# Optimization experiments

Measured on AMD Instinct MI355X. Metric: run time of the kernel, lower is better.

## Reference

```python
import jax, jax.numpy as jnp
import numpy as np

D_LATENT, D_HIDDEN, D_TIME, K = 128, 256, 16, 3
B, NX = 8, 4096
MSG_IN = 2 * D_LATENT + 1 + D_TIME + 2  # 275
UPD_IN = 2 * D_LATENT + D_TIME          # 272


def _gelu(v):
    return jax.nn.gelu(v, approximate=False)  # torch nn.GELU default (erf)


def _linear_params(key, din, dout):
    k1, k2 = jax.random.split(key)
    bound = 1.0 / np.sqrt(din)
    w = jax.random.uniform(k1, (din, dout), minval=-bound, maxval=bound, dtype=jnp.float32)
    b = jax.random.uniform(k2, (dout,), minval=-bound, maxval=bound, dtype=jnp.float32)
    return w, b


def setup_inputs() -> dict:
    key = jax.random.key(0)
    ks = jax.random.split(key, 16)
    inp = {
        'h': jax.random.normal(ks[0], (B, NX, D_LATENT), dtype=jnp.float32),
        'x': jax.random.uniform(ks[1], (B, NX), dtype=jnp.float32),
        'tau': jax.random.normal(ks[2], (B, D_TIME), dtype=jnp.float32),
        'u0': jax.random.normal(ks[3], (B, NX), dtype=jnp.float32),
    }
    inp['msg_w1'], inp['msg_b1'] = _linear_params(ks[4], MSG_IN, D_HIDDEN)
    inp['msg_w2'], inp['msg_b2'] = _linear_params(ks[5], D_HIDDEN, D_HIDDEN)
    inp['msg_w3'], inp['msg_b3'] = _linear_params(ks[6], D_HIDDEN, D_LATENT)
    inp['gate_w1'], inp['gate_b1'] = _linear_params(ks[7], MSG_IN, D_HIDDEN)
    inp['gate_w2'], inp['gate_b2'] = _linear_params(ks[8], D_HIDDEN, 1)
    inp['upd_w1'], inp['upd_b1'] = _linear_params(ks[9], UPD_IN, D_HIDDEN)
    inp['upd_w2'], inp['upd_b2'] = _linear_params(ks[10], D_HIDDEN, D_HIDDEN)
    inp['upd_w3'], inp['upd_b3'] = _linear_params(ks[11], D_HIDDEN, D_LATENT)
    inp['W_w'], inp['W_b'] = _linear_params(ks[12], D_LATENT, D_LATENT)
    return inp


def reference(h, x, tau, u0, msg_w1, msg_b1, msg_w2, msg_b2, msg_w3, msg_b3,
              gate_w1, gate_b1, gate_w2, gate_b2,
              upd_w1, upd_b1, upd_w2, upd_b2, upd_w3, upd_b3, W_w, W_b):
    Bq, nx, d = h.shape
    k = K
    S = 2 * k + 1
    # replicate padding along the spatial dim
    h_pad = jnp.pad(h, ((0, 0), (k, k), (0, 0)), mode='edge')
    x_pad = jnp.pad(x, ((0, 0), (k, k)), mode='edge')
    u0_pad = jnp.pad(u0, ((0, 0), (k, k)), mode='edge')
    # all stencil windows at once: idx[nx, S] gathers neighbor j for node i
    idx = jnp.arange(nx)[:, None] + jnp.arange(S)[None, :]
    h_j = h_pad[:, idx, :]                                  # [B, nx, S, d]
    rel = (x_pad[:, idx] - x[:, :, None])[..., None]        # [B, nx, S, 1]
    du0 = (u0[:, :, None] - u0_pad[:, idx])[..., None]      # [B, nx, S, 1]
    h_e = jnp.broadcast_to(h[:, :, None, :], (Bq, nx, S, d))
    tau_e = jnp.broadcast_to(tau[:, None, None, :], (Bq, nx, S, tau.shape[-1]))
    msg_in = jnp.concatenate([h_e, h_j, rel, tau_e, du0, jnp.abs(du0)], axis=-1)  # [B,nx,S,275]
    a = _gelu(msg_in @ msg_w1 + msg_b1)
    a = _gelu(a @ msg_w2 + msg_b2)
    msg = a @ msg_w3 + msg_b3                               # [B, nx, S, d]
    g = _gelu(msg_in @ gate_w1 + gate_b1)
    gate = jax.nn.sigmoid(g @ gate_w2 + gate_b2)            # [B, nx, S, 1]
    agg = jnp.sum(gate * msg, axis=2)                       # [B, nx, d]
    tau_n = jnp.broadcast_to(tau[:, None, :], (Bq, nx, tau.shape[-1]))
    upd_in = jnp.concatenate([h, agg, tau_n], axis=-1)      # [B, nx, 272]
    u = _gelu(upd_in @ upd_w1 + upd_b1)
    u = _gelu(u @ upd_w2 + upd_b2)
    h_nonlocal = u @ upd_w3 + upd_b3
    h_local = h @ W_w + W_b
    return _gelu(h_nonlocal + h_local)
```

## Files before the change

kernel.cpp:

```cpp
#include <hip/hip_runtime.h>
#include <hip/hip_bf16.h>
#include <math.h>

#define NXC 4096
#define NNODES 32768

typedef __attribute__((ext_vector_type(8))) short bf16x8;
typedef __attribute__((ext_vector_type(4))) short s16x4;
typedef __attribute__((ext_vector_type(16))) float f32x16;

#define MFMA32(a,b,c) __builtin_amdgcn_mfma_f32_32x32x16_bf16((a),(b),(c),0,0,0)

__device__ __forceinline__ float gelu_f(float v) {
    float z = v * fmaf(v*v, 0.10294324f, 2.3022082f);
    float e = __builtin_amdgcn_exp2f(z);
    return v - v * __builtin_amdgcn_rcpf(1.0f + e);
}
__device__ __forceinline__ float sigmoid_f(float v) {
    float e = __builtin_amdgcn_exp2f(-1.4426950409f * v);
    return __builtin_amdgcn_rcpf(1.0f + e);
}
__device__ __forceinline__ short f2bs(float x) {
    __hip_bfloat16 b = __float2bfloat16(x);
    union { __hip_bfloat16 h; short s; } u; u.h = b; return u.s;
}
__device__ __forceinline__ f32x16 zero16() {
    f32x16 v;
    #pragma unroll
    for (int i = 0; i < 16; ++i) v[i] = 0.f;
    return v;
}

__global__ void tau_kernel(const float* __restrict__ tau,
                           const float* __restrict__ msg_w1, const float* __restrict__ msg_b1,
                           const float* __restrict__ gate_w1, const float* __restrict__ gate_b1,
                           const float* __restrict__ upd_w1, const float* __restrict__ upd_b1,
                           float* __restrict__ TM, float* __restrict__ TG, float* __restrict__ TU)
{
    const int b = blockIdx.x;
    const int t = threadIdx.x;
    float tv[16];
    #pragma unroll
    for (int k = 0; k < 16; ++k) tv[k] = tau[b*16 + k];
    float am = msg_b1[t], ag = gate_b1[t], au = upd_b1[t];
    #pragma unroll
    for (int k = 0; k < 16; ++k) {
        am = fmaf(tv[k], msg_w1 [(257+k)*256 + t], am);
        ag = fmaf(tv[k], gate_w1[(257+k)*256 + t], ag);
        au = fmaf(tv[k], upd_w1 [(256+k)*256 + t], au);
    }
    TM[b*256+t] = am; TG[b*256+t] = ag; TU[b*256+t] = au;
}

__global__ void wconv_kernel(const float* __restrict__ msg_w2, const float* __restrict__ msg_w3,
                             const float* __restrict__ msg_w1, const float* __restrict__ gate_w1,
                             const float* __restrict__ upd_w1, const float* __restrict__ upd_w2,
                             const float* __restrict__ upd_w3, const float* __restrict__ W_w,
                             __hip_bfloat16* __restrict__ w2t, __hip_bfloat16* __restrict__ w3t,
                             __hip_bfloat16* __restrict__ wall_t, __hip_bfloat16* __restrict__ w1bt,
                             __hip_bfloat16* __restrict__ w2ut, __hip_bfloat16* __restrict__ w3ut)
{
    int i = blockIdx.x * 256 + threadIdx.x;
    if (i < 65536) { int c=i>>8, k=i&255; w2t[i] = __float2bfloat16(msg_w2[k*256+c]); return; }
    i -= 65536;
    if (i < 32768) { int c=i>>8, k=i&255; w3t[i] = __float2bfloat16(msg_w3[k*128+c]); return; }
    i -= 32768;
    if (i < 180224) {
        int c = i>>7, k = i&127; float v;
        if      (c <  256) v = msg_w1 [k*256 + c];
        else if (c <  512) v = msg_w1 [(128+k)*256 + (c-256)];
        else if (c <  768) v = gate_w1[k*256 + (c-512)];
        else if (c < 1024) v = gate_w1[(128+k)*256 + (c-768)];
        else if (c < 1280) v = upd_w1 [k*256 + (c-1024)];
        else               v = W_w    [k*128 + (c-1280)];
        wall_t[i] = __float2bfloat16(v); return;
    }
    i -= 180224;
    if (i < 32768) { int c=i>>7, k=i&127; w1bt[i] = __float2bfloat16(upd_w1[(128+k)*256+c]); return; }
    i -= 32768;
    if (i < 65536) { int c=i>>8, k=i&255; w2ut[i] = __float2bfloat16(upd_w2[k*256+c]); return; }
    i -= 65536;
    { int c=i>>8, k=i&255; w3ut[i] = __float2bfloat16(upd_w3[k*128+c]); }
}

#define PSTR 136

__global__ __launch_bounds__(256, 4)
void precompute_kernel(const float* __restrict__ h, const __hip_bfloat16* __restrict__ wall_t,
                       const float* __restrict__ W_b,
                       __hip_bfloat16* __restrict__ PAm, __hip_bfloat16* __restrict__ PBm,
                       __hip_bfloat16* __restrict__ PAg, __hip_bfloat16* __restrict__ PBg,
                       __hip_bfloat16* __restrict__ HU, float* __restrict__ HL)
{
    __shared__ __align__(16) __hip_bfloat16 hs[64*PSTR];
    const int t = threadIdx.x;
    const int lane = t & 63, wv = t >> 6;
    const int cl = lane & 31, g = lane >> 5;
    const int base = blockIdx.x * 64;
    const int tile = blockIdx.y;

    #pragma unroll
    for (int i = 0; i < 8; ++i) {
        int f = (i*256 + t)*4;
        float4 hv = *(const float4*)&h[(size_t)base*128 + f];
        int row = f >> 7, col = f & 127;
        s16x4 pk; pk[0]=f2bs(hv.x); pk[1]=f2bs(hv.y); pk[2]=f2bs(hv.z); pk[3]=f2bs(hv.w);
        *(s16x4*)&hs[row*PSTR + col] = pk;
    }
    __syncthreads();

    f32x16 acc0 = zero16(), acc1 = zero16();
    {
        const __hip_bfloat16* wp  = wall_t + ((size_t)tile*128 + wv*32 + cl)*128 + g*8;
        const __hip_bfloat16* a0  = hs + (size_t)(cl)*PSTR + g*8;
        const __hip_bfloat16* a1p = hs + (size_t)(32+cl)*PSTR + g*8;
        #pragma unroll
        for (int kt = 0; kt < 8; ++kt) {
            bf16x8 bf = *(const bf16x8*)(wp + kt*16);
            acc0 = MFMA32(*(const bf16x8*)(a0  + kt*16), bf, acc0);
            acc1 = MFMA32(*(const bf16x8*)(a1p + kt*16), bf, acc1);
        }
    }
    if (tile < 10) {
        __syncthreads();
        __hip_bfloat16* ob = hs;
        const int ncol = wv*32 + cl;
        #pragma unroll
        for (int r = 0; r < 16; ++r) {
            int row = (r&3) + 8*(r>>2) + 4*g;
            ob[row*128 + ncol]      = __float2bfloat16(acc0[r]);
            ob[(32+row)*128 + ncol] = __float2bfloat16(acc1[r]);
        }
        __syncthreads();
        __hip_bfloat16* bufs[5] = {PAm, PBm, PAg, PBg, HU};
        __hip_bfloat16* dst = bufs[tile >> 1];
        const int coloff = (tile & 1) * 128;
        #pragma unroll
        for (int i = 0; i < 4; ++i) {
            int idx = i*256 + t;
            int row = idx >> 4, ch = idx & 15;
            *(float4*)&dst[(size_t)(base+row)*256 + coloff + ch*8] =
                *(const float4*)&ob[row*128 + ch*8];
        }
    } else {
        const int col = (wv*32 + cl) & 127;
        float wb = W_b[col];
        #pragma unroll
        for (int r = 0; r < 16; ++r) {
            int row = (r&3) + 8*(r>>2) + 4*g;
            HL[(size_t)(base+row)*128 + col]    = acc0[r] + wb;
            HL[(size_t)(base+32+row)*128 + col] = acc1[r] + wb;
        }
    }
}

#define ENPB 8
#define EEPB 56
#define ARS  264
#define MRS  132

__global__ __launch_bounds__(256, 4)
void edge_kernel(const float* __restrict__ x, const float* __restrict__ u0,
                 const float* __restrict__ msg_w1, const float* __restrict__ gate_w1,
                 const __hip_bfloat16* __restrict__ w2t, const float* __restrict__ msg_b2,
                 const __hip_bfloat16* __restrict__ w3t, const float* __restrict__ msg_b3,
                 const float* __restrict__ gate_w2, const float* __restrict__ gate_b2,
                 const __hip_bfloat16* __restrict__ PAm, const __hip_bfloat16* __restrict__ PBm,
                 const __hip_bfloat16* __restrict__ PAg, const __hip_bfloat16* __restrict__ PBg,
                 const float* __restrict__ TM, const float* __restrict__ TG,
                 float* __restrict__ AGG)
{
    __shared__ __align__(16) __hip_bfloat16 act[64*ARS];
    __shared__ float s_gp[4][EEPB];
    __shared__ float s_rel[EEPB], s_du[EEPB], s_ad[EEPB];
    __shared__ int   s_slotj[14];
    __shared__ float s_gate[EEPB];

    const int t    = threadIdx.x;
    const int lane = t & 63;
    const int wv   = t >> 6;
    const int base = blockIdx.x * ENPB;
    const int b    = base >> 12;
    const int ii0  = base & (NXC-1);

    if (t < 14) {
        int jj = ii0 - 3 + t;
        jj = jj < 0 ? 0 : (jj > NXC-1 ? NXC-1 : jj);
        s_slotj[t] = b*NXC + jj;
    }
    if (t < EEPB) {
        int nd = t / 7, s = t - nd*7;
        int i  = base + nd;
        int jj = ii0 + nd + s - 3;
        jj = jj < 0 ? 0 : (jj > NXC-1 ? NXC-1 : jj);
        int j = b*NXC + jj;
        float rel = x[j] - x[i];
        float du  = u0[i] - u0[j];
        s_rel[t] = rel; s_du[t] = du; s_ad[t] = fabsf(du);
    }
    __syncthreads();

    {
        float wr  = msg_w1 [256*256+t], wd  = msg_w1 [273*256+t], wa  = msg_w1 [274*256+t];
        float gwr = gate_w1[256*256+t], gwd = gate_w1[273*256+t], gwa = gate_w1[274*256+t];
        float tm = TM[b*256+t], tg = TG[b*256+t];
        float g2 = gate_w2[t];
        float bm[14], bg[14], pam[8], pag[8];
        #pragma unroll
        for (int q = 0; q < 14; ++q) {
            size_t o = (size_t)s_slotj[q]*256 + t;
            bm[q] = __bfloat162float(PBm[o]) + tm;
            bg[q] = __bfloat162float(PBg[o]) + tg;
        }
        #pragma unroll
        for (int nd = 0; nd < 8; ++nd) {
            size_t o = (size_t)(base+nd)*256 + t;
            pam[nd] = __bfloat162float(PAm[o]);
            pag[nd] = __bfloat162float(PAg[o]);
        }
        #pragma unroll
        for (int nd = 0; nd < 8; ++nd) {
            #pragma unroll
            for (int s = 0; s < 7; ++s) {
                const int e = nd*7 + s, q = nd + s;
                float rel = s_rel[e], du = s_du[e], ad = s_ad[e];
                float pm = pam[nd] + bm[q];
                pm = fmaf(rel, wr, pm); pm = fmaf(du, wd, pm); pm = fmaf(ad, wa, pm);
                act[e*ARS + t] = __float2bfloat16(gelu_f(pm));
                float pg = pag[nd] + bg[q];
                pg = fmaf(rel, gwr, pg); pg = fmaf(du, gwd, pg); pg = fmaf(ad, gwa, pg);
                float gv = gelu_f(pg) * g2;
                #pragma unroll
                for (int off = 32; off > 0; off >>= 1) gv += __shfl_xor(gv, off);
                if (lane == 0) s_gp[wv][e] = gv;
            }
        }
    }
    __syncthreads();
    if (t < EEPB)
        s_gate[t] = sigmoid_f(s_gp[0][t] + s_gp[1][t] + s_gp[2][t] + s_gp[3][t] + gate_b2[0]);

    const int cl = lane & 31;
    const int g  = lane >> 5;
    f32x16 acc00 = zero16(), acc01 = zero16(), acc10 = zero16(), acc11 = zero16();
    {
        const __hip_bfloat16* w2a = w2t + (size_t)((wv*2+0)*32 + cl)*256 + g*8;
        const __hip_bfloat16* w2b = w2t + (size_t)((wv*2+1)*32 + cl)*256 + g*8;
        const __hip_bfloat16* a1a = act + (size_t)(cl)*ARS + g*8;
        const __hip_bfloat16* a1b = act + (size_t)(32+cl)*ARS + g*8;
        #pragma unroll
        for (int kt = 0; kt < 16; ++kt) {
            bf16x8 bfa = *(const bf16x8*)(w2a + kt*16);
            bf16x8 bfb = *(const bf16x8*)(w2b + kt*16);
            bf16x8 afa = *(const bf16x8*)(a1a + kt*16);
            bf16x8 afb = *(const bf16x8*)(a1b + kt*16);
            acc00 = MFMA32(afa, bfa, acc00);
            acc01 = MFMA32(afa, bfb, acc01);
            acc10 = MFMA32(afb, bfa, acc10);
            acc11 = MFMA32(afb, bfb, acc11);
        }
    }
    __syncthreads();
    {
        const int c0 = (wv*2+0)*32 + cl;
        const int c1 = (wv*2+1)*32 + cl;
        float b20 = msg_b2[c0], b21 = msg_b2[c1];
        #pragma unroll
        for (int r = 0; r < 16; ++r) {
            int row0 = (r&3) + 8*(r>>2) + 4*g;
            int row1 = 32 + row0;
            act[row0*ARS + c0] = __float2bfloat16(gelu_f(acc00[r] + b20));
            act[row0*ARS + c1] = __float2bfloat16(gelu_f(acc01[r] + b21));
            act[row1*ARS + c0] = __float2bfloat16(gelu_f(acc10[r] + b20));
            act[row1*ARS + c1] = __float2bfloat16(gelu_f(acc11[r] + b21));
        }
    }
    __syncthreads();

    f32x16 m0 = zero16(), m1 = zero16();
    {
        const __hip_bfloat16* w3p = w3t + (size_t)(wv*32 + cl)*256 + g*8;
        const __hip_bfloat16* a2a = act + (size_t)(cl)*ARS + g*8;
        const __hip_bfloat16* a2b = act + (size_t)(32+cl)*ARS + g*8;
        #pragma unroll
        for (int kt = 0; kt < 16; ++kt) {
            bf16x8 bfr = *(const bf16x8*)(w3p + kt*16);
            m0 = MFMA32(*(const bf16x8*)(a2a + kt*16), bfr, m0);
            m1 = MFMA32(*(const bf16x8*)(a2b + kt*16), bfr, m1);
        }
    }
    __syncthreads();
    float* msgbuf = (float*)act;
    {
        const int c = wv*32 + cl;
        float b3v = msg_b3[c];
        #pragma unroll
        for (int r = 0; r < 16; ++r) {
            int row0 = (r&3) + 8*(r>>2) + 4*g;
            int row1 = 32 + row0;
            msgbuf[row0*MRS + c] = (m0[r] + b3v) * s_gate[row0];
            if (row1 < EEPB)
                msgbuf[row1*MRS + c] = (m1[r] + b3v) * s_gate[row1];
        }
    }
    __syncthreads();

    {
        const int c   = t & 127;
        const int grp = t >> 7;
        #pragma unroll
        for (int p = 0; p < 4; ++p) {
            int nd = grp + p*2;
            float ssum = 0.f;
            #pragma unroll
            for (int q2 = 0; q2 < 7; ++q2) ssum += msgbuf[(nd*7+q2)*MRS + c];
            AGG[(size_t)(base+nd)*128 + c] = ssum;
        }
    }
}

#define UM 32

__global__ __launch_bounds__(256, 4)
void update_kernel(const __hip_bfloat16* __restrict__ w1bt, const __hip_bfloat16* __restrict__ w2ut,
                   const __hip_bfloat16* __restrict__ w3ut,
                   const float* __restrict__ upd_b2, const float* __restrict__ upd_b3,
                   const __hip_bfloat16* __restrict__ HU, const float* __restrict__ HL,
                   const float* __restrict__ AGG, const float* __restrict__ TU,
                   float* __restrict__ out)
{
    __shared__ __align__(16) __hip_bfloat16 ub[UM*ARS];
    const int t = threadIdx.x;
    const int lane = t & 63, wv = t >> 6;
    const int cl = lane & 31, g = lane >> 5;
    const int base = blockIdx.x * UM;
    const int b = base >> 12;

    #pragma unroll
    for (int i = 0; i < 4; ++i) {
        int f = (i*256 + t)*4;
        float4 av = *(const float4*)&AGG[(size_t)base*128 + f];
        int row = f >> 7, col = f & 127;
        s16x4 pk; pk[0]=f2bs(av.x); pk[1]=f2bs(av.y); pk[2]=f2bs(av.z); pk[3]=f2bs(av.w);
        *(s16x4*)&ub[row*ARS + col] = pk;
    }
    __syncthreads();

    f32x16 u0a = zero16(), u1a = zero16();
    {
        const __hip_bfloat16* a0 = ub + (size_t)(cl)*ARS + g*8;
        const __hip_bfloat16* b0 = w1bt + (size_t)(wv*64 + cl)*128 + g*8;
        const __hip_bfloat16* b1 = w1bt + (size_t)(wv*64 + 32 + cl)*128 + g*8;
        #pragma unroll
        for (int kt = 0; kt < 8; ++kt) {
            bf16x8 af = *(const bf16x8*)(a0 + kt*16);
            u0a = MFMA32(af, *(const bf16x8*)(b0 + kt*16), u0a);
            u1a = MFMA32(af, *(const bf16x8*)(b1 + kt*16), u1a);
        }
    }
    __syncthreads();
    {
        const int c0 = wv*64 + cl, c1 = c0 + 32;
        float tu0 = TU[b*256 + c0], tu1 = TU[b*256 + c1];
        #pragma unroll
        for (int r = 0; r < 16; ++r) {
            int row = (r&3) + 8*(r>>2) + 4*g;
            int n0 = base + row;
            ub[row*ARS + c0] = __float2bfloat16(gelu_f(u0a[r] + tu0 + __bfloat162float(HU[(size_t)n0*256 + c0])));
            ub[row*ARS + c1] = __float2bfloat16(gelu_f(u1a[r] + tu1 + __bfloat162float(HU[(size_t)n0*256 + c1])));
        }
    }
    __syncthreads();

    f32x16 v0a = zero16(), v1a = zero16();
    {
        const __hip_bfloat16* a0 = ub + (size_t)(cl)*ARS + g*8;
        const __hip_bfloat16* b0 = w2ut + (size_t)(wv*64 + cl)*256 + g*8;
        const __hip_bfloat16* b1 = w2ut + (size_t)(wv*64 + 32 + cl)*256 + g*8;
        #pragma unroll
        for (int kt = 0; kt < 16; ++kt) {
            bf16x8 af = *(const bf16x8*)(a0 + kt*16);
            v0a = MFMA32(af, *(const bf16x8*)(b0 + kt*16), v0a);
            v1a = MFMA32(af, *(const bf16x8*)(b1 + kt*16), v1a);
        }
    }
    __syncthreads();
    {
        const int c0 = wv*64 + cl, c1 = c0 + 32;
        float b20 = upd_b2[c0], b21 = upd_b2[c1];
        #pragma unroll
        for (int r = 0; r < 16; ++r) {
            int row = (r&3) + 8*(r>>2) + 4*g;
            ub[row*ARS + c0] = __float2bfloat16(gelu_f(v0a[r] + b20));
            ub[row*ARS + c1] = __float2bfloat16(gelu_f(v1a[r] + b21));
        }
    }
    __syncthreads();

    f32x16 w0a = zero16();
    {
        const __hip_bfloat16* wp = w3ut + (size_t)(wv*32 + cl)*256 + g*8;
        const __hip_bfloat16* a0 = ub + (size_t)(cl)*ARS + g*8;
        #pragma unroll
        for (int kt = 0; kt < 16; ++kt)
            w0a = MFMA32(*(const bf16x8*)(a0 + kt*16), *(const bf16x8*)(wp + kt*16), w0a);
    }
    {
        const int c = wv*32 + cl;
        float b3v = upd_b3[c];
        #pragma unroll
        for (int r = 0; r < 16; ++r) {
            int row = (r&3) + 8*(r>>2) + 4*g;
            size_t o = (size_t)(base+row)*128 + c;
            out[o] = gelu_f(w0a[r] + b3v + HL[o]);
        }
    }
}

extern "C" void kernel_launch(void* const* d_in, const int* in_sizes, int n_in,
                              void* d_out, int out_size, void* d_ws, size_t ws_size,
                              hipStream_t stream)
{
    const float* h      = (const float*)d_in[0];
    const float* x      = (const float*)d_in[1];
    const float* tau    = (const float*)d_in[2];
    const float* u0     = (const float*)d_in[3];
    const float* msg_w1 = (const float*)d_in[4];
    const float* msg_b1 = (const float*)d_in[5];
    const float* msg_w2 = (const float*)d_in[6];
    const float* msg_b2 = (const float*)d_in[7];
    const float* msg_w3 = (const float*)d_in[8];
    const float* msg_b3 = (const float*)d_in[9];
    const float* gate_w1= (const float*)d_in[10];
    const float* gate_b1= (const float*)d_in[11];
    const float* gate_w2= (const float*)d_in[12];
    const float* gate_b2= (const float*)d_in[13];
    const float* upd_w1 = (const float*)d_in[14];
    const float* upd_b1 = (const float*)d_in[15];
    const float* upd_w2 = (const float*)d_in[16];
    const float* upd_b2 = (const float*)d_in[17];
    const float* upd_w3 = (const float*)d_in[18];
    const float* upd_b3 = (const float*)d_in[19];
    const float* W_w    = (const float*)d_in[20];
    const float* W_b    = (const float*)d_in[21];
    float* out = (float*)d_out;

    char* ws = (char*)d_ws;
    size_t off = 0;
    auto alloc = [&](size_t bytes) -> void* {
        void* p = ws + off;
        off += (bytes + 255) & ~(size_t)255;
        return p;
    };
    __hip_bfloat16* PAm = (__hip_bfloat16*)alloc((size_t)NNODES*256*2);
    __hip_bfloat16* PBm = (__hip_bfloat16*)alloc((size_t)NNODES*256*2);
    __hip_bfloat16* PAg = (__hip_bfloat16*)alloc((size_t)NNODES*256*2);
    __hip_bfloat16* PBg = (__hip_bfloat16*)alloc((size_t)NNODES*256*2);
    __hip_bfloat16* HU  = (__hip_bfloat16*)alloc((size_t)NNODES*256*2);
    float* HL  = (float*)alloc((size_t)NNODES*128*4);
    float* AGG = (float*)alloc((size_t)NNODES*128*4);
    float* TM  = (float*)alloc(8*256*4);
    float* TG  = (float*)alloc(8*256*4);
    float* TU  = (float*)alloc(8*256*4);
    __hip_bfloat16* w2t   = (__hip_bfloat16*)alloc((size_t)256*256*2);
    __hip_bfloat16* w3t   = (__hip_bfloat16*)alloc((size_t)128*256*2);
    __hip_bfloat16* wall_t= (__hip_bfloat16*)alloc((size_t)1408*128*2);
    __hip_bfloat16* w1bt  = (__hip_bfloat16*)alloc((size_t)256*128*2);
    __hip_bfloat16* w2ut  = (__hip_bfloat16*)alloc((size_t)256*256*2);
    __hip_bfloat16* w3ut  = (__hip_bfloat16*)alloc((size_t)128*256*2);
    (void)ws_size; (void)in_sizes; (void)n_in; (void)out_size;

    tau_kernel<<<8, 256, 0, stream>>>(tau, msg_w1, msg_b1, gate_w1, gate_b1,
                                      upd_w1, upd_b1, TM, TG, TU);
    wconv_kernel<<<1600, 256, 0, stream>>>(msg_w2, msg_w3, msg_w1, gate_w1,
                                           upd_w1, upd_w2, upd_w3, W_w,
                                           w2t, w3t, wall_t, w1bt, w2ut, w3ut);
    precompute_kernel<<<dim3(NNODES/64, 11), 256, 0, stream>>>(h, wall_t, W_b,
                                                               PAm, PBm, PAg, PBg, HU, HL);
    edge_kernel<<<NNODES/ENPB, 256, 0, stream>>>(x, u0, msg_w1, gate_w1,
                                                 w2t, msg_b2, w3t, msg_b3,
                                                 gate_w2, gate_b2,
                                                 PAm, PBm, PAg, PBg, TM, TG, AGG);
    update_kernel<<<NNODES/UM, 256, 0, stream>>>(w1bt, w2ut, w3ut, upd_b2, upd_b3,
                                                 HU, HL, AGG, TU, out);
}
```

Measured before the change: 240.6 us.

## Fuse h projections into update kernel and batch gate reductions with DPP

The upd_w1 h-part and W_w local projections move out of precompute into update_kernel, which now loads h and AGG into LDS and runs a K=256 matmul plus the W_w product. This removes the HU and HL intermediate buffers and their global round-trip. Precompute now computes 4 wider tiles (256 columns, 4 accumulators per wave) instead of 11 narrower ones. The edge kernel replaces one full 6-step shuffle reduction per edge with a DPP transpose-reduce over groups of 4 edges, and it skips stores for padding rows beyond 56.

```diff
diff --git a/kernel.cpp b/kernel.cpp
--- a/kernel.cpp
+++ b/kernel.cpp
@@ -29,6 +29,12 @@
     #pragma unroll
     for (int i = 0; i < 16; ++i) v[i] = 0.f;
     return v;
+}
+__device__ __forceinline__ float dpp_xor1(float x) {
+    return __int_as_float(__builtin_amdgcn_update_dpp(0, __float_as_int(x), 0xB1, 0xF, 0xF, true));
+}
+__device__ __forceinline__ float dpp_xor2(float x) {
+    return __int_as_float(__builtin_amdgcn_update_dpp(0, __float_as_int(x), 0x4E, 0xF, 0xF, true));
 }
 
 __global__ void tau_kernel(const float* __restrict__ tau,
@@ -57,42 +63,41 @@
                              const float* __restrict__ upd_w1, const float* __restrict__ upd_w2,
                              const float* __restrict__ upd_w3, const float* __restrict__ W_w,
                              __hip_bfloat16* __restrict__ w2t, __hip_bfloat16* __restrict__ w3t,
-                             __hip_bfloat16* __restrict__ wall_t, __hip_bfloat16* __restrict__ w1bt,
-                             __hip_bfloat16* __restrict__ w2ut, __hip_bfloat16* __restrict__ w3ut)
+                             __hip_bfloat16* __restrict__ wall_t, __hip_bfloat16* __restrict__ w1ut,
+                             __hip_bfloat16* __restrict__ w2ut, __hip_bfloat16* __restrict__ w3ut,
+                             __hip_bfloat16* __restrict__ wwt)
 {
     int i = blockIdx.x * 256 + threadIdx.x;
     if (i < 65536) { int c=i>>8, k=i&255; w2t[i] = __float2bfloat16(msg_w2[k*256+c]); return; }
     i -= 65536;
     if (i < 32768) { int c=i>>8, k=i&255; w3t[i] = __float2bfloat16(msg_w3[k*128+c]); return; }
     i -= 32768;
-    if (i < 180224) {
+    if (i < 131072) {
         int c = i>>7, k = i&127; float v;
         if      (c <  256) v = msg_w1 [k*256 + c];
         else if (c <  512) v = msg_w1 [(128+k)*256 + (c-256)];
         else if (c <  768) v = gate_w1[k*256 + (c-512)];
-        else if (c < 1024) v = gate_w1[(128+k)*256 + (c-768)];
-        else if (c < 1280) v = upd_w1 [k*256 + (c-1024)];
-        else               v = W_w    [k*128 + (c-1280)];
+        else               v = gate_w1[(128+k)*256 + (c-768)];
         wall_t[i] = __float2bfloat16(v); return;
     }
-    i -= 180224;
-    if (i < 32768) { int c=i>>7, k=i&127; w1bt[i] = __float2bfloat16(upd_w1[(128+k)*256+c]); return; }
-    i -= 32768;
+    i -= 131072;
+    if (i < 65536) { int c=i>>8, k=i&255; w1ut[i] = __float2bfloat16(upd_w1[k*256+c]); return; }
+    i -= 65536;
     if (i < 65536) { int c=i>>8, k=i&255; w2ut[i] = __float2bfloat16(upd_w2[k*256+c]); return; }
     i -= 65536;
-    { int c=i>>8, k=i&255; w3ut[i] = __float2bfloat16(upd_w3[k*128+c]); }
+    if (i < 32768) { int c=i>>8, k=i&255; w3ut[i] = __float2bfloat16(upd_w3[k*128+c]); return; }
+    i -= 32768;
+    { int c=i>>7, k=i&127; wwt[i] = __float2bfloat16(W_w[k*128+c]); }
 }
 
 #define PSTR 136
 
 __global__ __launch_bounds__(256, 4)
 void precompute_kernel(const float* __restrict__ h, const __hip_bfloat16* __restrict__ wall_t,
-                       const float* __restrict__ W_b,
                        __hip_bfloat16* __restrict__ PAm, __hip_bfloat16* __restrict__ PBm,
-                       __hip_bfloat16* __restrict__ PAg, __hip_bfloat16* __restrict__ PBg,
-                       __hip_bfloat16* __restrict__ HU, float* __restrict__ HL)
+                       __hip_bfloat16* __restrict__ PAg, __hip_bfloat16* __restrict__ PBg)
 {
-    __shared__ __align__(16) __hip_bfloat16 hs[64*PSTR];
+    __shared__ __align__(16) __hip_bfloat16 lds[64*256];
     const int t = threadIdx.x;
     const int lane = t & 63, wv = t >> 6;
     const int cl = lane & 31, g = lane >> 5;
@@ -105,51 +110,51 @@
         float4 hv = *(const float4*)&h[(size_t)base*128 + f];
         int row = f >> 7, col = f & 127;
         s16x4 pk; pk[0]=f2bs(hv.x); pk[1]=f2bs(hv.y); pk[2]=f2bs(hv.z); pk[3]=f2bs(hv.w);
-        *(s16x4*)&hs[row*PSTR + col] = pk;
-    }
-    __syncthreads();
-
-    f32x16 acc0 = zero16(), acc1 = zero16();
-    {
-        const __hip_bfloat16* wp  = wall_t + ((size_t)tile*128 + wv*32 + cl)*128 + g*8;
-        const __hip_bfloat16* a0  = hs + (size_t)(cl)*PSTR + g*8;
-        const __hip_bfloat16* a1p = hs + (size_t)(32+cl)*PSTR + g*8;
+        *(s16x4*)&lds[row*PSTR + col] = pk;
+    }
+    __syncthreads();
+
+    f32x16 a00 = zero16(), a01 = zero16(), a10 = zero16(), a11 = zero16();
+    {
+        const int c0 = wv*64 + cl, c1 = c0 + 32;
+        const __hip_bfloat16* b0 = wall_t + ((size_t)tile*256 + c0)*128 + g*8;
+        const __hip_bfloat16* b1 = wall_t + ((size_t)tile*256 + c1)*128 + g*8;
+        const __hip_bfloat16* a0 = lds + (size_t)(cl)*PSTR + g*8;
+        const __hip_bfloat16* a1p = lds + (size_t)(32+cl)*PSTR + g*8;
         #pragma unroll
         for (int kt = 0; kt < 8; ++kt) {
-            bf16x8 bf = *(const bf16x8*)(wp + kt*16);
-            acc0 = MFMA32(*(const bf16x8*)(a0  + kt*16), bf, acc0);
-            acc1 = MFMA32(*(const bf16x8*)(a1p + kt*16), bf, acc1);
-        }
-    }
-    if (tile < 10) {
-        __syncthreads();
-        __hip_bfloat16* ob = hs;
-        const int ncol = wv*32 + cl;
+            bf16x8 bf0 = *(const bf16x8*)(b0 + kt*16);
+            bf16x8 bf1 = *(const bf16x8*)(b1 + kt*16);
+            bf16x8 af0 = *(const bf16x8*)(a0 + kt*16);
+            bf16x8 af1 = *(const bf16x8*)(a1p + kt*16);
+            a00 = MFMA32(af0, bf0, a00);
+            a01 = MFMA32(af0, bf1, a01);
+            a10 = MFMA32(af1, bf0, a10);
+            a11 = MFMA32(af1, bf1, a11);
+        }
+    }
+    __syncthreads();
+    {
+        const int c0 = wv*64 + cl, c1 = c0 + 32;
         #pragma unroll
         for (int r = 0; r < 16; ++r) {
             int row = (r&3) + 8*(r>>2) + 4*g;
-            ob[row*128 + ncol]      = __float2bfloat16(acc0[r]);
-            ob[(32+row)*128 + ncol] = __float2bfloat16(acc1[r]);
-        }
-        __syncthreads();
-        __hip_bfloat16* bufs[5] = {PAm, PBm, PAg, PBg, HU};
-        __hip_bfloat16* dst = bufs[tile >> 1];
-        const int coloff = (tile & 1) * 128;
-        #pragma unroll
-        for (int i = 0; i < 4; ++i) {
+            lds[row*256 + c0]      = __float2bfloat16(a00[r]);
+            lds[row*256 + c1]      = __float2bfloat16(a01[r]);
+            lds[(32+row)*256 + c0] = __float2bfloat16(a10[r]);
+            lds[(32+row)*256 + c1] = __float2bfloat16(a11[r]);
+        }
+    }
+    __syncthreads();
+    {
+        __hip_bfloat16* bufs[4] = {PAm, PBm, PAg, PBg};
+        __hip_bfloat16* dst = bufs[tile];
+        #pragma unroll
+        for (int i = 0; i < 8; ++i) {
             int idx = i*256 + t;
-            int row = idx >> 4, ch = idx & 15;
-            *(float4*)&dst[(size_t)(base+row)*256 + coloff + ch*8] =
-                *(const float4*)&ob[row*128 + ch*8];
-        }
-    } else {
-        const int col = (wv*32 + cl) & 127;
-        float wb = W_b[col];
-        #pragma unroll
-        for (int r = 0; r < 16; ++r) {
-            int row = (r&3) + 8*(r>>2) + 4*g;
-            HL[(size_t)(base+row)*128 + col]    = acc0[r] + wb;
-            HL[(size_t)(base+32+row)*128 + col] = acc1[r] + wb;
+            int row = idx >> 5, ch = idx & 31;
+            *(float4*)&dst[(size_t)(base+row)*256 + ch*8] =
+                *(const float4*)&lds[row*256 + ch*8];
         }
     }
 }
@@ -205,7 +210,7 @@
         float gwr = gate_w1[256*256+t], gwd = gate_w1[273*256+t], gwa = gate_w1[274*256+t];
         float tm = TM[b*256+t], tg = TG[b*256+t];
         float g2 = gate_w2[t];
-        float bm[14], bg[14], pam[8], pag[8];
+        float bm[14], bg[14], pam[8], pag[8], sacc[14];
         #pragma unroll
         for (int q = 0; q < 14; ++q) {
             size_t o = (size_t)s_slotj[q]*256 + t;
@@ -218,22 +223,38 @@
             pam[nd] = __bfloat162float(PAm[o]);
             pag[nd] = __bfloat162float(PAg[o]);
         }
-        #pragma unroll
-        for (int nd = 0; nd < 8; ++nd) {
+        const bool p1 = (lane & 1), p2 = ((lane & 2) != 0);
+        #pragma unroll
+        for (int m = 0; m < 14; ++m) {
+            float gq[4];
             #pragma unroll
-            for (int s = 0; s < 7; ++s) {
-                const int e = nd*7 + s, q = nd + s;
+            for (int r4i = 0; r4i < 4; ++r4i) {
+                const int e = m*4 + r4i;
+                const int nd = e / 7, s = e - nd*7, q = nd + s;
                 float rel = s_rel[e], du = s_du[e], ad = s_ad[e];
                 float pm = pam[nd] + bm[q];
                 pm = fmaf(rel, wr, pm); pm = fmaf(du, wd, pm); pm = fmaf(ad, wa, pm);
                 act[e*ARS + t] = __float2bfloat16(gelu_f(pm));
                 float pg = pag[nd] + bg[q];
                 pg = fmaf(rel, gwr, pg); pg = fmaf(du, gwd, pg); pg = fmaf(ad, gwa, pg);
-                float gv = gelu_f(pg) * g2;
-                #pragma unroll
-                for (int off = 32; off > 0; off >>= 1) gv += __shfl_xor(gv, off);
-                if (lane == 0) s_gp[wv][e] = gv;
+                gq[r4i] = gelu_f(pg) * g2;
             }
+            float xx = p1 ? gq[1] : gq[0], yy = p1 ? gq[0] : gq[1];
+            xx += dpp_xor1(yy);
+            float zz = p1 ? gq[3] : gq[2], ww = p1 ? gq[2] : gq[3];
+            zz += dpp_xor1(ww);
+            float uu = p2 ? zz : xx, vv = p2 ? xx : zz;
+            uu += dpp_xor2(vv);
+            sacc[m] = uu;
+        }
+        #pragma unroll
+        for (int m = 0; m < 14; ++m) {
+            float v = sacc[m];
+            v += __shfl_xor(v, 4);
+            v += __shfl_xor(v, 8);
+            v += __shfl_xor(v, 16);
+            v += __shfl_xor(v, 32);
+            if (lane < 4) s_gp[wv][m*4 + lane] = v;
         }
     }
     __syncthreads();
@@ -268,11 +289,13 @@
         #pragma unroll
         for (int r = 0; r < 16; ++r) {
             int row0 = (r&3) + 8*(r>>2) + 4*g;
-            int row1 = 32 + row0;
             act[row0*ARS + c0] = __float2bfloat16(gelu_f(acc00[r] + b20));
             act[row0*ARS + c1] = __float2bfloat16(gelu_f(acc01[r] + b21));
-            act[row1*ARS + c0] = __float2bfloat16(gelu_f(acc10[r] + b20));
-            act[row1*ARS + c1] = __float2bfloat16(gelu_f(acc11[r] + b21));
+            if (r < 12) {
+                int row1 = 32 + row0;
+                act[row1*ARS + c0] = __float2bfloat16(gelu_f(acc10[r] + b20));
+                act[row1*ARS + c1] = __float2bfloat16(gelu_f(acc11[r] + b21));
+            }
         }
     }
     __syncthreads();
@@ -322,11 +345,12 @@
 #define UM 32
 
 __global__ __launch_bounds__(256, 4)
-void update_kernel(const __hip_bfloat16* __restrict__ w1bt, const __hip_bfloat16* __restrict__ w2ut,
-                   const __hip_bfloat16* __restrict__ w3ut,
+void update_kernel(const __hip_bfloat16* __restrict__ w1ut, const __hip_bfloat16* __restrict__ w2ut,
+                   const __hip_bfloat16* __restrict__ w3ut, const __hip_bfloat16* __restrict__ wwt,
                    const float* __restrict__ upd_b2, const float* __restrict__ upd_b3,
-                   const __hip_bfloat16* __restrict__ HU, const float* __restrict__ HL,
-                   const float* __restrict__ AGG, const float* __restrict__ TU,
+                   const float* __restrict__ W_b,
+                   const float* __restrict__ h, const float* __restrict__ AGG,
+                   const float* __restrict__ TU,
                    float* __restrict__ out)
 {
     __shared__ __align__(16) __hip_bfloat16 ub[UM*ARS];
@@ -339,23 +363,29 @@
     #pragma unroll
     for (int i = 0; i < 4; ++i) {
         int f = (i*256 + t)*4;
+        int row = f >> 7, col = f & 127;
+        float4 hv = *(const float4*)&h[(size_t)base*128 + f];
+        s16x4 pk; pk[0]=f2bs(hv.x); pk[1]=f2bs(hv.y); pk[2]=f2bs(hv.z); pk[3]=f2bs(hv.w);
+        *(s16x4*)&ub[row*ARS + col] = pk;
         float4 av = *(const float4*)&AGG[(size_t)base*128 + f];
-        int row = f >> 7, col = f & 127;
-        s16x4 pk; pk[0]=f2bs(av.x); pk[1]=f2bs(av.y); pk[2]=f2bs(av.z); pk[3]=f2bs(av.w);
-        *(s16x4*)&ub[row*ARS + col] = pk;
-    }
-    __syncthreads();
-
-    f32x16 u0a = zero16(), u1a = zero16();
+        s16x4 pa; pa[0]=f2bs(av.x); pa[1]=f2bs(av.y); pa[2]=f2bs(av.z); pa[3]=f2bs(av.w);
+        *(s16x4*)&ub[row*ARS + 128 + col] = pa;
+    }
+    __syncthreads();
+
+    f32x16 u0a = zero16(), u1a = zero16(), hl = zero16();
     {
         const __hip_bfloat16* a0 = ub + (size_t)(cl)*ARS + g*8;
-        const __hip_bfloat16* b0 = w1bt + (size_t)(wv*64 + cl)*128 + g*8;
-        const __hip_bfloat16* b1 = w1bt + (size_t)(wv*64 + 32 + cl)*128 + g*8;
-        #pragma unroll
-        for (int kt = 0; kt < 8; ++kt) {
+        const __hip_bfloat16* b0 = w1ut + (size_t)(wv*64 + cl)*256 + g*8;
+        const __hip_bfloat16* b1 = w1ut + (size_t)(wv*64 + 32 + cl)*256 + g*8;
+        const __hip_bfloat16* bw = wwt + (size_t)(wv*32 + cl)*128 + g*8;
+        #pragma unroll
+        for (int kt = 0; kt < 16; ++kt) {
             bf16x8 af = *(const bf16x8*)(a0 + kt*16);
             u0a = MFMA32(af, *(const bf16x8*)(b0 + kt*16), u0a);
             u1a = MFMA32(af, *(const bf16x8*)(b1 + kt*16), u1a);
+            if (kt < 8)
+                hl = MFMA32(af, *(const bf16x8*)(bw + kt*16), hl);
         }
     }
     __syncthreads();
@@ -365,9 +395,8 @@
         #pragma unroll
         for (int r = 0; r < 16; ++r) {
             int row = (r&3) + 8*(r>>2) + 4*g;
-            int n0 = base + row;
-            ub[row*ARS + c0] = __float2bfloat16(gelu_f(u0a[r] + tu0 + __bfloat162float(HU[(size_t)n0*256 + c0])));
-            ub[row*ARS + c1] = __float2bfloat16(gelu_f(u1a[r] + tu1 + __bfloat162float(HU[(size_t)n0*256 + c1])));
+            ub[row*ARS + c0] = __float2bfloat16(gelu_f(u0a[r] + tu0));
+            ub[row*ARS + c1] = __float2bfloat16(gelu_f(u1a[r] + tu1));
         }
     }
     __syncthreads();
@@ -407,12 +436,12 @@
     }
     {
         const int c = wv*32 + cl;
-        float b3v = upd_b3[c];
+        float b3v = upd_b3[c] + W_b[c];
         #pragma unroll
         for (int r = 0; r < 16; ++r) {
             int row = (r&3) + 8*(r>>2) + 4*g;
             size_t o = (size_t)(base+row)*128 + c;
-            out[o] = gelu_f(w0a[r] + b3v + HL[o]);
+            out[o] = gelu_f(w0a[r] + b3v + hl[r]);
         }
     }
 }
@@ -456,31 +485,31 @@
     __hip_bfloat16* PBm = (__hip_bfloat16*)alloc((size_t)NNODES*256*2);
     __hip_bfloat16* PAg = (__hip_bfloat16*)alloc((size_t)NNODES*256*2);
     __hip_bfloat16* PBg = (__hip_bfloat16*)alloc((size_t)NNODES*256*2);
-    __hip_bfloat16* HU  = (__hip_bfloat16*)alloc((size_t)NNODES*256*2);
-    float* HL  = (float*)alloc((size_t)NNODES*128*4);
     float* AGG = (float*)alloc((size_t)NNODES*128*4);
     float* TM  = (float*)alloc(8*256*4);
     float* TG  = (float*)alloc(8*256*4);
     float* TU  = (float*)alloc(8*256*4);
     __hip_bfloat16* w2t   = (__hip_bfloat16*)alloc((size_t)256*256*2);
     __hip_bfloat16* w3t   = (__hip_bfloat16*)alloc((size_t)128*256*2);
-    __hip_bfloat16* wall_t= (__hip_bfloat16*)alloc((size_t)1408*128*2);
-    __hip_bfloat16* w1bt  = (__hip_bfloat16*)alloc((size_t)256*128*2);
+    __hip_bfloat16* wall_t= (__hip_bfloat16*)alloc((size_t)1024*128*2);
+    __hip_bfloat16* w1ut  = (__hip_bfloat16*)alloc((size_t)256*256*2);
     __hip_bfloat16* w2ut  = (__hip_bfloat16*)alloc((size_t)256*256*2);
     __hip_bfloat16* w3ut  = (__hip_bfloat16*)alloc((size_t)128*256*2);
+    __hip_bfloat16* wwt   = (__hip_bfloat16*)alloc((size_t)128*128*2);
     (void)ws_size; (void)in_sizes; (void)n_in; (void)out_size;
 
     tau_kernel<<<8, 256, 0, stream>>>(tau, msg_w1, msg_b1, gate_w1, gate_b1,
                                       upd_w1, upd_b1, TM, TG, TU);
     wconv_kernel<<<1600, 256, 0, stream>>>(msg_w2, msg_w3, msg_w1, gate_w1,
                                            upd_w1, upd_w2, upd_w3, W_w,
-                                           w2t, w3t, wall_t, w1bt, w2ut, w3ut);
-    precompute_kernel<<<dim3(NNODES/64, 11), 256, 0, stream>>>(h, wall_t, W_b,
-                                                               PAm, PBm, PAg, PBg, HU, HL);
+                                           w2t, w3t, wall_t, w1ut, w2ut, w3ut, wwt);
+    precompute_kernel<<<dim3(NNODES/64, 4), 256, 0, stream>>>(h, wall_t,
+                                                              PAm, PBm, PAg, PBg);
     edge_kernel<<<NNODES/ENPB, 256, 0, stream>>>(x, u0, msg_w1, gate_w1,
                                                  w2t, msg_b2, w3t, msg_b3,
                                                  gate_w2, gate_b2,
                                                  PAm, PBm, PAg, PBg, TM, TG, AGG);
-    update_kernel<<<NNODES/UM, 256, 0, stream>>>(w1bt, w2ut, w3ut, upd_b2, upd_b3,
-                                                 HU, HL, AGG, TU, out);
-}
+    update_kernel<<<NNODES/UM, 256, 0, stream>>>(w1ut, w2ut, w3ut, wwt,
+                                                 upd_b2, upd_b3, W_b,
+                                                 h, AGG, TU, out);
+}
```

Result: faster. 205.0 us (-14.8%).
